# Kernel optimization log

Measured on AMD Instinct MI355X. Metric: run time of the kernel, lower is better.

## Reference

```python
import jax, jax.numpy as jnp
import numpy as np

TAU = 0.1
NEG = -1000000.0

def setup_inputs() -> dict:
    key = jax.random.key(0)
    x = jax.random.normal(key, (16, 2048, 512), dtype=jnp.float32)
    return {"x": x}

def reference(x):
    # x: [B, S, D]
    d = x.shape[-1]
    scores = jnp.einsum('bsd,btd->bst', x, x) / jnp.sqrt(jnp.asarray(d, x.dtype))
    scores = jnp.where(scores > TAU, scores, jnp.asarray(NEG, x.dtype))
    weights = jax.nn.softmax(scores, axis=-1)          # [B, S, S]
    context = jnp.einsum('bst,btd->bsd', weights, x)   # [B, S, D]
    return (context, weights)
```

## Files before the change

### kernel.cpp

```cpp
#include <hip/hip_runtime.h>
#include <hip/hip_bf16.h>
#include <stdint.h>

#define B_ 16
#define S_ 2048
#define D_ 512
#define TAU 0.1f
#define SCALE 0.04419417382415922f
#define BM 128
#define BN 32

typedef __attribute__((ext_vector_type(8))) __bf16 bf16x8;
typedef __attribute__((ext_vector_type(4))) float f32x4;
typedef __attribute__((ext_vector_type(16))) float f32x16;
typedef __attribute__((ext_vector_type(8))) uint16_t u16x8;
typedef __attribute__((ext_vector_type(4))) uint16_t u16x4;

__device__ __forceinline__ uint16_t f2bf(float f) {
  __hip_bfloat16 h = __float2bfloat16(f);
  return __builtin_bit_cast(uint16_t, h);
}

__device__ __forceinline__ float bf2f(uint16_t u) {
  return __uint_as_float(((uint32_t)u) << 16);
}

__device__ __forceinline__ void g2lds16(void* lds, const void* g) {
  __builtin_amdgcn_global_load_lds(
      (const __attribute__((address_space(1))) unsigned int*)g,
      (__attribute__((address_space(3))) unsigned int*)lds, 16, 0, 0);
}

__global__ __launch_bounds__(256) void convert_kernel(
    const float* __restrict__ x, uint16_t* __restrict__ xbf,
    uint16_t* __restrict__ xt) {
  const int bid = blockIdx.x;
  const int b = bid >> 8;
  const int tt = (bid >> 3) & 31;
  const int dt = bid & 7;
  const int t0 = tt * 64, d0 = dt * 64;
  __shared__ uint16_t tile[64][72];
  const int tid = threadIdx.x;
  const float* xb = x + ((size_t)b * S_ + t0) * D_ + d0;

#pragma unroll
  for (int it = 0; it < 4; ++it) {
    int r = it * 16 + (tid >> 4);
    int c = (tid & 15) * 4;
    float4 v = *(const float4*)(xb + (size_t)r * D_ + c);
    tile[r][c + 0] = f2bf(v.x);
    tile[r][c + 1] = f2bf(v.y);
    tile[r][c + 2] = f2bf(v.z);
    tile[r][c + 3] = f2bf(v.w);
  }
  __syncthreads();

#pragma unroll
  for (int it = 0; it < 2; ++it) {
    int G = it * 256 + tid;
    int tl = G >> 3, gl = G & 7;
    int t = t0 + tl;
    int p = (d0 >> 3) + (gl ^ (t & 7));
    u16x8 v = *(const u16x8*)&tile[tl][gl * 8];
    *(u16x8*)((char*)xbf + (size_t)(b * S_ + t) * 1024 + p * 16) = v;
  }
#pragma unroll
  for (int it = 0; it < 2; ++it) {
    int G = it * 256 + tid;
    int dl = G >> 3, gl = G & 7;
    int d = d0 + dl;
    int p = (gl & ~3) | ((gl ^ (d & 3)) & 3);
    u16x8 v;
#pragma unroll
    for (int i = 0; i < 8; ++i) v[i] = tile[gl * 8 + i][dl];
    *(u16x8*)((char*)xt + (size_t)(b * D_ + d) * 4096 + t0 * 2 + p * 16) = v;
  }
}

__global__ __launch_bounds__(512, 2) void attn_scores(
    const uint16_t* __restrict__ xbf, uint16_t* __restrict__ E,
    float* __restrict__ psum_g) {
  __shared__ uint16_t klds[64 * 512];
  __shared__ uint16_t wlds[4 * 32 * 64];
  __shared__ float redbuf[4 * 2 * 32];

  const int tid = threadIdx.x;
  const int wave = tid >> 6, lane = tid & 63;
  const int h = lane >> 5, l31 = lane & 31, l7 = lane & 7;
  const int qi = wave >> 1, ki = wave & 1;
  const int bid = blockIdx.x;
  const int job = (bid & 7) * 32 + (bid >> 3);
  const int b = job >> 4;
  const int q0 = (job & 15) * BM;

  const char* xb = (const char*)xbf + (size_t)b * S_ * 1024;
  const char* kldsc = (const char*)klds;
  char* wldsc = (char*)wlds;

  const size_t qrow = (size_t)(q0 + qi * 32 + l31);
  bf16x8 qf[32];
#pragma unroll
  for (int s = 0; s < 32; ++s) {
    int g = (2 * s + h) ^ l7;
    qf[s] = *(const bf16x8*)(xb + qrow * 1024 + g * 16);
  }

  float psum = 0.f;

  for (int kt = 0; kt < 32; ++kt) {
#pragma unroll
    for (int i = 0; i < 8; ++i) {
      int row = wave * 8 + i;
      g2lds16((char*)klds + row * 1024,
              xb + (size_t)(kt * 64 + row) * 1024 + lane * 16);
    }
    __syncthreads();

    f32x16 acc = {};
#pragma unroll
    for (int s = 0; s < 32; ++s) {
      int g = (2 * s + h) ^ l7;
      bf16x8 af = *(const bf16x8*)(kldsc + (size_t)(ki * 32 + l31) * 1024 + g * 16);
      acc = __builtin_amdgcn_mfma_f32_32x32x16_bf16(af, qf[s], acc, 0, 0, 0);
    }

#pragma unroll
    for (int rp = 0; rp < 8; ++rp) {
      int r = 2 * rp;
      float s0 = acc[r] * SCALE;
      float s1 = acc[r + 1] * SCALE;
      float e0 = (s0 > TAU) ? __expf(s0) : 0.f;
      float e1 = (s1 > TAU) ? __expf(s1) : 0.f;
      psum += e0 + e1;
      int k0 = ki * 32 + (r & 3) + 8 * (r >> 2) + 4 * h;
      int slot = (k0 >> 3) ^ l7;
      uint32_t pk = (uint32_t)f2bf(e0) | ((uint32_t)f2bf(e1) << 16);
      *(uint32_t*)(wldsc + qi * 4096 + l31 * 128 + slot * 16 + (k0 & 7) * 2) = pk;
    }
    __syncthreads();

#pragma unroll
    for (int j = 0; j < 2; ++j) {
      int ql = ki * 16 + j * 8 + (lane >> 3);
      u16x8 v = *(const u16x8*)(wldsc + qi * 4096 + ql * 128 + ((l7 ^ (ql & 7)) * 16));
      *(u16x8*)(E + ((size_t)(b * S_ + q0 + qi * 32 + ql)) * 2048 + kt * 64 + l7 * 8) = v;
    }
  }

  psum += __shfl_xor(psum, 32, 64);
  if (lane < 32) redbuf[qi * 64 + ki * 32 + lane] = psum;
  __syncthreads();
  if (ki == 0 && lane < 32) {
    float tot = redbuf[qi * 64 + lane] + redbuf[qi * 64 + 32 + lane];
    psum_g[(size_t)b * S_ + q0 + qi * 32 + lane] = tot;
  }
}

__global__ __launch_bounds__(512) void attn_pv3(
    const uint16_t* __restrict__ E, const uint16_t* __restrict__ xt,
    const float* __restrict__ psum_g, float* __restrict__ ctx,
    float* __restrict__ wout) {
  __shared__ uint16_t xtlds[2][512 * 64];
  __shared__ uint16_t wstage[128 * 64];
  __shared__ float invlds[128];

  const int tid = threadIdx.x;
  const int wave = tid >> 6, lane = tid & 63;
  const int h = lane >> 5, l31 = lane & 31, l7 = lane & 7;
  const int qi = wave >> 1, di = wave & 1;
  const int bid = blockIdx.x;
  const int job = (bid & 7) * 32 + (bid >> 3);
  const int b = job >> 4;
  const int q0 = (job & 15) * BM;

  const char* xtb = (const char*)xt + (size_t)b * D_ * 4096;
  char* wstc = (char*)wstage;

  const float inv = 1.0f / psum_g[(size_t)b * S_ + q0 + qi * 32 + l31];
  if (tid < 128) invlds[tid] = 1.0f / psum_g[(size_t)b * S_ + q0 + tid];

#pragma unroll
  for (int i = 0; i < 8; ++i) {
    int d = wave * 64 + i * 8 + (lane >> 3);
    int gd = l7 ^ (d & 7);
    int p2 = (gd & ~3) | ((gd ^ (d & 3)) & 3);
    g2lds16((char*)xtlds[0] + (wave * 64 + i * 8) * 128,
            xtb + (size_t)d * 4096 + p2 * 16);
  }
  __syncthreads();

  f32x16 pv[8];
#pragma unroll
  for (int t = 0; t < 8; ++t) pv[t] = (f32x16){};

  const uint16_t* Erow =
      E + ((size_t)(b * S_ + q0 + qi * 32 + l31)) * 2048 + 8 * h;

  for (int kt = 0; kt < 32; ++kt) {
    const int cur = kt & 1;
    const char* xcur = (const char*)xtlds[cur];

    if (kt < 31) {
#pragma unroll
      for (int i = 0; i < 8; ++i) {
        int d = wave * 64 + i * 8 + (lane >> 3);
        int gd = l7 ^ (d & 7);
        int p2 = (gd & ~3) | ((gd ^ (d & 3)) & 3);
        g2lds16((char*)xtlds[cur ^ 1] + (wave * 64 + i * 8) * 128,
                xtb + (size_t)d * 4096 + (kt + 1) * 128 + p2 * 16);
      }
    }

    bf16x8 bfr[4];
#pragma unroll
    for (int ks = 0; ks < 4; ++ks) {
      bfr[ks] = *(const bf16x8*)(Erow + kt * 64 + 16 * ks);
    }

#pragma unroll
    for (int t = 0; t < 8; ++t) {
      int dl = di * 256 + t * 32 + l31;
#pragma unroll
      for (int ks = 0; ks < 4; ++ks) {
        int slot = (2 * ks + h) ^ (dl & 7);
        bf16x8 af = *(const bf16x8*)(xcur + (size_t)dl * 128 + slot * 16);
        pv[t] = __builtin_amdgcn_mfma_f32_32x32x16_bf16(af, bfr[ks], pv[t], 0, 0, 0);
      }
    }

    if (di == 0) {
      int q = qi * 32 + l31;
#pragma unroll
      for (int ks = 0; ks < 4; ++ks) {
        int g = (2 * ks + h) ^ (q & 7);
        *(u16x8*)(wstc + q * 128 + g * 16) = __builtin_bit_cast(u16x8, bfr[ks]);
      }
    }
    __syncthreads();

#pragma unroll
    for (int j = 0; j < 2; ++j) {
      int row = wave * 16 + j * 8 + (lane >> 3);
      float invq = invlds[row];
#pragma unroll
      for (int half = 0; half < 2; ++half) {
        int g = (half * 4 + (l7 >> 1)) ^ (row & 7);
        u16x4 ev = *(const u16x4*)(wstc + row * 128 + g * 16 + (l7 & 1) * 8);
        f32x4 w;
#pragma unroll
        for (int i = 0; i < 4; ++i) w[i] = bf2f(ev[i]) * invq;
        *(f32x4*)(wout + ((size_t)(b * S_ + q0 + row)) * 2048 + kt * 64 +
                  half * 32 + l7 * 4) = w;
      }
    }
    __syncthreads();
  }

  char* sbuf = (char*)xtlds[0] + wave * 4096;
#pragma unroll
  for (int t = 0; t < 8; ++t) {
#pragma unroll
    for (int rp = 0; rp < 8; ++rp) {
      int r = 2 * rp;
      int d0 = (r & 3) + 8 * (r >> 2) + 4 * h;
      int g = (d0 >> 2) ^ (l31 & 7);
      float2 v = make_float2(pv[t][r] * inv, pv[t][r + 1] * inv);
      *(float2*)(sbuf + l31 * 128 + g * 16 + (d0 & 3) * 4) = v;
    }
#pragma unroll
    for (int jj = 0; jj < 4; ++jj) {
      int row = jj * 8 + (lane >> 3);
      int g = l7 ^ (row & 7);
      f32x4 vv = *(const f32x4*)(sbuf + row * 128 + g * 16);
      *(f32x4*)(ctx + ((size_t)(b * S_ + q0 + qi * 32 + row)) * 512 +
                di * 256 + t * 32 + l7 * 4) = vv;
    }
  }
}

__global__ __launch_bounds__(512, 2) void attn_main(
    const uint16_t* __restrict__ xbf, const uint16_t* __restrict__ xtr,
    float* __restrict__ ctx, float* __restrict__ wout) {
  __shared__ uint16_t klds[BN * D_];
  __shared__ uint16_t xtlds[D_ * BN];
  __shared__ uint16_t wlds[8][16][40];

  const int tid = threadIdx.x;
  const int wave = tid >> 6, lane = tid & 63;
  const int lg = lane >> 4, lr = lane & 15;
  const int bid = blockIdx.x;
  const int job = (bid & 7) * 32 + (bid >> 3);
  const int b = job >> 4;
  const int q0 = (job & 15) * BM;

  const char* xb = (const char*)(xbf + (size_t)b * S_ * D_);
  const char* xtb = (const char*)(xtr + (size_t)b * D_ * S_);

  const int qrow = q0 + wave * 16 + lr;
  bf16x8 qf[16];
#pragma unroll
  for (int c = 0; c < 16; ++c) {
    int g = (4 * c + lg) ^ (qrow & 7);
    qf[c] = *(const bf16x8*)(xb + (size_t)qrow * 1024 + g * 16);
  }

  float psum[4] = {0.f, 0.f, 0.f, 0.f};

  for (int kt = 0; kt < S_ / BN; ++kt) {
    const char* ksrc = xb + (size_t)kt * BN * 1024;
#pragma unroll
    for (int it = 0; it < 4; ++it) {
      int ob = it * 8192 + wave * 1024;
      g2lds16((char*)klds + ob, ksrc + ob + lane * 16);
    }
    __syncthreads();
    f32x4 acc0 = {0.f, 0.f, 0.f, 0.f}, acc1 = {0.f, 0.f, 0.f, 0.f};
#pragma unroll
    for (int c = 0; c < 16; ++c) {
      {
        int t = lr;
        int g = (4 * c + lg) ^ (t & 7);
        bf16x8 bf = *(const bf16x8*)((const char*)klds + t * 1024 + g * 16);
        acc0 = __builtin_amdgcn_mfma_f32_16x16x32_bf16(qf[c], bf, acc0, 0, 0, 0);
      }
      {
        int t = 16 + lr;
        int g = (4 * c + lg) ^ (t & 7);
        bf16x8 bf = *(const bf16x8*)((const char*)klds + t * 1024 + g * 16);
        acc1 = __builtin_amdgcn_mfma_f32_16x16x32_bf16(qf[c], bf, acc1, 0, 0, 0);
      }
    }
#pragma unroll
    for (int r = 0; r < 4; ++r) {
      float s0 = acc0[r] * SCALE;
      float s1 = acc1[r] * SCALE;
      psum[r] += (s0 > TAU ? __expf(s0) : 0.f) + (s1 > TAU ? __expf(s1) : 0.f);
    }
    __syncthreads();
  }

#pragma unroll
  for (int r = 0; r < 4; ++r) {
    float v = psum[r];
#pragma unroll
    for (int m = 1; m < 16; m <<= 1) v += __shfl_xor(v, m, 64);
    psum[r] = 1.f / v;
  }

  f32x4 pv[32];
  const f32x4 fz = {0.f, 0.f, 0.f, 0.f};
#pragma unroll
  for (int n = 0; n < 32; ++n) pv[n] = fz;

  for (int kt = 0; kt < S_ / BN; ++kt) {
    const char* ksrc = xb + (size_t)kt * BN * 1024;
#pragma unroll
    for (int it = 0; it < 4; ++it) {
      int ob = it * 8192 + wave * 1024;
      g2lds16((char*)klds + ob, ksrc + ob + lane * 16);
    }
#pragma unroll
    for (int it = 0; it < 4; ++it) {
      int ob = it * 8192 + wave * 1024;
      int o = ob + lane * 16;
      const char* src = xtb + (size_t)(o >> 6) * 4096 + kt * 64 + (o & 63);
      g2lds16((char*)xtlds + ob, src);
    }
    __syncthreads();

    f32x4 acc0 = {0.f, 0.f, 0.f, 0.f}, acc1 = {0.f, 0.f, 0.f, 0.f};
#pragma unroll
    for (int c = 0; c < 16; ++c) {
      {
        int t = lr;
        int g = (4 * c + lg) ^ (t & 7);
        bf16x8 bf = *(const bf16x8*)((const char*)klds + t * 1024 + g * 16);
        acc0 = __builtin_amdgcn_mfma_f32_16x16x32_bf16(qf[c], bf, acc0, 0, 0, 0);
      }
      {
        int t = 16 + lr;
        int g = (4 * c + lg) ^ (t & 7);
        bf16x8 bf = *(const bf16x8*)((const char*)klds + t * 1024 + g * 16);
        acc1 = __builtin_amdgcn_mfma_f32_16x16x32_bf16(qf[c], bf, acc1, 0, 0, 0);
      }
    }

#pragma unroll
    for (int j = 0; j < 2; ++j) {
      f32x4 a = j ? acc1 : acc0;
#pragma unroll
      for (int r = 0; r < 4; ++r) {
        float s = a[r] * SCALE;
        float w = (s > TAU) ? __expf(s) * psum[r] : 0.f;
        int ql = wave * 16 + 4 * lg + r;
        wout[((size_t)(b * S_ + q0 + ql)) * S_ + kt * BN + j * 16 + lr] = w;
        wlds[wave][4 * lg + r][j * 16 + lr] = f2bf(w);
      }
    }

    bf16x8 wa = *(const bf16x8*)((const char*)&wlds[wave][0][0] + lr * 80 + lg * 16);
#pragma unroll
    for (int n = 0; n < 32; ++n) {
      int d = n * 16 + lr;
      int g = lg ^ (d & 3);
      bf16x8 bf = *(const bf16x8*)((const char*)xtlds + d * 64 + g * 16);
      pv[n] = __builtin_amdgcn_mfma_f32_16x16x32_bf16(wa, bf, pv[n], 0, 0, 0);
    }
    __syncthreads();
  }

  const int qg = q0 + wave * 16 + 4 * lg;
#pragma unroll
  for (int n = 0; n < 32; ++n) {
#pragma unroll
    for (int r = 0; r < 4; ++r) {
      ctx[((size_t)(b * S_ + qg + r)) * D_ + n * 16 + lr] = pv[n][r];
    }
  }
}

__global__ __launch_bounds__(256) void fb_weights(const float* __restrict__ x,
                                                  float* __restrict__ wout) {
  const int b = blockIdx.x >> 11;
  const int q = blockIdx.x & 2047;
  __shared__ float qv[512];
  __shared__ float red[256];
  const int tid = threadIdx.x;
  const float* xb = x + (size_t)b * S_ * D_;
  for (int d = tid; d < 512; d += 256) qv[d] = xb[(size_t)q * 512 + d];
  __syncthreads();
  float s[8];
  float lsum = 0.f;
#pragma unroll
  for (int i = 0; i < 8; ++i) {
    int k = i * 256 + tid;
    const float* xr = xb + (size_t)k * 512;
    float dot = 0.f;
    for (int d = 0; d < 512; ++d) dot += qv[d] * xr[d];
    dot *= SCALE;
    float e = (dot > TAU) ? __expf(dot) : 0.f;
    s[i] = e;
    lsum += e;
  }
  red[tid] = lsum;
  __syncthreads();
  for (int st = 128; st > 0; st >>= 1) {
    if (tid < st) red[tid] += red[tid + st];
    __syncthreads();
  }
  float inv = 1.f / red[0];
#pragma unroll
  for (int i = 0; i < 8; ++i)
    wout[((size_t)(b * S_ + q)) * S_ + i * 256 + tid] = s[i] * inv;
}

__global__ __launch_bounds__(256) void fb_ctx(const float* __restrict__ x,
                                              const float* __restrict__ wout,
                                              float* __restrict__ ctx) {
  const int b = blockIdx.x >> 11;
  const int q = blockIdx.x & 2047;
  const int tid = threadIdx.x;
  const float* xb = x + (size_t)b * S_ * D_;
  const float* wr = wout + ((size_t)(b * S_ + q)) * S_;
  float a0 = 0.f, a1 = 0.f;
  for (int k = 0; k < 2048; ++k) {
    float w = wr[k];
    a0 += w * xb[(size_t)k * 512 + tid];
    a1 += w * xb[(size_t)k * 512 + 256 + tid];
  }
  ctx[((size_t)(b * S_ + q)) * 512 + tid] = a0;
  ctx[((size_t)(b * S_ + q)) * 512 + 256 + tid] = a1;
}

extern "C" void kernel_launch(void* const* d_in, const int* in_sizes, int n_in,
                              void* d_out, int out_size, void* d_ws, size_t ws_size,
                              hipStream_t stream) {
  (void)in_sizes; (void)n_in; (void)out_size;
  const float* x = (const float*)d_in[0];
  float* ctx = (float*)d_out;
  float* wout = (float*)d_out + (size_t)B_ * S_ * D_;

  const size_t half = (size_t)B_ * S_ * D_ * 2;
  const size_t e_bytes = (size_t)B_ * S_ * S_ * 2;
  const size_t psum_bytes = (size_t)B_ * S_ * 4;
  const size_t need_new = 2 * half + e_bytes + psum_bytes;

  if (ws_size >= need_new) {
    uint16_t* xbf = (uint16_t*)d_ws;
    uint16_t* xtr = (uint16_t*)((char*)d_ws + half);
    uint16_t* E = (uint16_t*)((char*)d_ws + 2 * half);
    float* psum_g = (float*)((char*)d_ws + 2 * half + e_bytes);
    convert_kernel<<<dim3(4096), dim3(256), 0, stream>>>(x, xbf, xtr);
    attn_scores<<<dim3(256), dim3(512), 0, stream>>>(xbf, E, psum_g);
    attn_pv3<<<dim3(256), dim3(512), 0, stream>>>(E, xtr, psum_g, ctx, wout);
  } else if (ws_size >= 2 * half) {
    uint16_t* xbf = (uint16_t*)d_ws;
    uint16_t* xtr = (uint16_t*)((char*)d_ws + half);
    convert_kernel<<<dim3(4096), dim3(256), 0, stream>>>(x, xbf, xtr);
    attn_main<<<dim3(256), dim3(512), 0, stream>>>(xbf, xtr, ctx, wout);
  } else {
    fb_weights<<<dim3(32768), dim3(256), 0, stream>>>(x, wout);
    fb_ctx<<<dim3(32768), dim3(256), 0, stream>>>(x, wout, ctx);
  }
}
```

Before: 292.7 us.

## Double-buffer K tiles in scores, write E and weights directly from registers

The scores kernel now double-buffers the K tile in LDS, prefetching the next tile during the MFMAs, and writes the bf16 exp values straight from accumulator registers to global memory instead of staging them through LDS. This removes one barrier and an LDS round trip per iteration. The PV kernel is remapped so each wave computes two 32-row query groups over 128 d columns, reusing each LDS A-fragment for two MFMAs. It writes normalized weights and context directly from registers without LDS staging. The direct global writes are narrower (8–16 byte) and less coalesced, and the register-held accumulators and fragments grow with the two-per-SM occupancy hint.

```diff
diff --git a/kernel.cpp b/kernel.cpp
--- a/kernel.cpp
+++ b/kernel.cpp
@@ -80,8 +80,7 @@
 __global__ __launch_bounds__(512, 2) void attn_scores(
     const uint16_t* __restrict__ xbf, uint16_t* __restrict__ E,
     float* __restrict__ psum_g) {
-  __shared__ uint16_t klds[64 * 512];
-  __shared__ uint16_t wlds[4 * 32 * 64];
+  __shared__ uint16_t klds[2][64 * 512];
   __shared__ float redbuf[4 * 2 * 32];
 
   const int tid = threadIdx.x;
@@ -94,8 +93,6 @@
   const int q0 = (job & 15) * BM;
 
   const char* xb = (const char*)xbf + (size_t)b * S_ * 1024;
-  const char* kldsc = (const char*)klds;
-  char* wldsc = (char*)wlds;
 
   const size_t qrow = (size_t)(q0 + qi * 32 + l31);
   bf16x8 qf[32];
@@ -107,14 +104,25 @@
 
   float psum = 0.f;
 
+#pragma unroll
+  for (int i = 0; i < 8; ++i) {
+    int row = wave * 8 + i;
+    g2lds16((char*)klds[0] + row * 1024, xb + (size_t)row * 1024 + lane * 16);
+  }
+  __syncthreads();
+
   for (int kt = 0; kt < 32; ++kt) {
-#pragma unroll
-    for (int i = 0; i < 8; ++i) {
-      int row = wave * 8 + i;
-      g2lds16((char*)klds + row * 1024,
-              xb + (size_t)(kt * 64 + row) * 1024 + lane * 16);
-    }
-    __syncthreads();
+    const int cur = kt & 1;
+    const char* kldsc = (const char*)klds[cur];
+
+    if (kt < 31) {
+#pragma unroll
+      for (int i = 0; i < 8; ++i) {
+        int row = wave * 8 + i;
+        g2lds16((char*)klds[cur ^ 1] + row * 1024,
+                xb + (size_t)((kt + 1) * 64 + row) * 1024 + lane * 16);
+      }
+    }
 
     f32x16 acc = {};
 #pragma unroll
@@ -124,27 +132,20 @@
       acc = __builtin_amdgcn_mfma_f32_32x32x16_bf16(af, qf[s], acc, 0, 0, 0);
     }
 
-#pragma unroll
-    for (int rp = 0; rp < 8; ++rp) {
-      int r = 2 * rp;
-      float s0 = acc[r] * SCALE;
-      float s1 = acc[r + 1] * SCALE;
-      float e0 = (s0 > TAU) ? __expf(s0) : 0.f;
-      float e1 = (s1 > TAU) ? __expf(s1) : 0.f;
-      psum += e0 + e1;
-      int k0 = ki * 32 + (r & 3) + 8 * (r >> 2) + 4 * h;
-      int slot = (k0 >> 3) ^ l7;
-      uint32_t pk = (uint32_t)f2bf(e0) | ((uint32_t)f2bf(e1) << 16);
-      *(uint32_t*)(wldsc + qi * 4096 + l31 * 128 + slot * 16 + (k0 & 7) * 2) = pk;
-    }
-    __syncthreads();
-
-#pragma unroll
-    for (int j = 0; j < 2; ++j) {
-      int ql = ki * 16 + j * 8 + (lane >> 3);
-      u16x8 v = *(const u16x8*)(wldsc + qi * 4096 + ql * 128 + ((l7 ^ (ql & 7)) * 16));
-      *(u16x8*)(E + ((size_t)(b * S_ + q0 + qi * 32 + ql)) * 2048 + kt * 64 + l7 * 8) = v;
-    }
+    uint16_t* ep = E + ((size_t)b * S_ + qrow) * 2048 + kt * 64 + ki * 32 + 4 * h;
+#pragma unroll
+    for (int q4 = 0; q4 < 4; ++q4) {
+      u16x4 w4;
+#pragma unroll
+      for (int j = 0; j < 4; ++j) {
+        float s = acc[4 * q4 + j] * SCALE;
+        float e = (s > TAU) ? __expf(s) : 0.f;
+        psum += e;
+        w4[j] = f2bf(e);
+      }
+      *(u16x4*)(ep + 8 * q4) = w4;
+    }
+    __syncthreads();
   }
 
   psum += __shfl_xor(psum, 32, 64);
@@ -156,28 +157,32 @@
   }
 }
 
-__global__ __launch_bounds__(512) void attn_pv3(
+__global__ __launch_bounds__(512, 2) void attn_pv5(
     const uint16_t* __restrict__ E, const uint16_t* __restrict__ xt,
     const float* __restrict__ psum_g, float* __restrict__ ctx,
     float* __restrict__ wout) {
   __shared__ uint16_t xtlds[2][512 * 64];
-  __shared__ uint16_t wstage[128 * 64];
-  __shared__ float invlds[128];
 
   const int tid = threadIdx.x;
   const int wave = tid >> 6, lane = tid & 63;
   const int h = lane >> 5, l31 = lane & 31, l7 = lane & 7;
-  const int qi = wave >> 1, di = wave & 1;
+  const int qi = wave & 1, di = wave >> 1;
   const int bid = blockIdx.x;
   const int job = (bid & 7) * 32 + (bid >> 3);
   const int b = job >> 4;
   const int q0 = (job & 15) * BM;
 
   const char* xtb = (const char*)xt + (size_t)b * D_ * 4096;
-  char* wstc = (char*)wstage;
-
-  const float inv = 1.0f / psum_g[(size_t)b * S_ + q0 + qi * 32 + l31];
-  if (tid < 128) invlds[tid] = 1.0f / psum_g[(size_t)b * S_ + q0 + tid];
+
+  float invq[2];
+#pragma unroll
+  for (int qg = 0; qg < 2; ++qg)
+    invq[qg] = 1.0f / psum_g[(size_t)b * S_ + q0 + qi * 64 + qg * 32 + l31];
+
+  const uint16_t* Erow[2];
+#pragma unroll
+  for (int qg = 0; qg < 2; ++qg)
+    Erow[qg] = E + ((size_t)(b * S_ + q0 + qi * 64 + qg * 32 + l31)) * 2048 + 8 * h;
 
 #pragma unroll
   for (int i = 0; i < 8; ++i) {
@@ -189,12 +194,11 @@
   }
   __syncthreads();
 
-  f32x16 pv[8];
-#pragma unroll
-  for (int t = 0; t < 8; ++t) pv[t] = (f32x16){};
-
-  const uint16_t* Erow =
-      E + ((size_t)(b * S_ + q0 + qi * 32 + l31)) * 2048 + 8 * h;
+  f32x16 pv[2][4];
+#pragma unroll
+  for (int qg = 0; qg < 2; ++qg)
+#pragma unroll
+    for (int t = 0; t < 4; ++t) pv[qg][t] = (f32x16){};
 
   for (int kt = 0; kt < 32; ++kt) {
     const int cur = kt & 1;
@@ -211,69 +215,57 @@
       }
     }
 
-    bf16x8 bfr[4];
-#pragma unroll
-    for (int ks = 0; ks < 4; ++ks) {
-      bfr[ks] = *(const bf16x8*)(Erow + kt * 64 + 16 * ks);
-    }
-
-#pragma unroll
-    for (int t = 0; t < 8; ++t) {
-      int dl = di * 256 + t * 32 + l31;
+    bf16x8 bfr[2][4];
+#pragma unroll
+    for (int qg = 0; qg < 2; ++qg)
+#pragma unroll
+      for (int ks = 0; ks < 4; ++ks)
+        bfr[qg][ks] = *(const bf16x8*)(Erow[qg] + kt * 64 + 16 * ks);
+
+#pragma unroll
+    for (int t = 0; t < 4; ++t) {
+      const int dl = di * 128 + t * 32 + l31;
 #pragma unroll
       for (int ks = 0; ks < 4; ++ks) {
-        int slot = (2 * ks + h) ^ (dl & 7);
+        int slot = (2 * ks + h) ^ l7;
         bf16x8 af = *(const bf16x8*)(xcur + (size_t)dl * 128 + slot * 16);
-        pv[t] = __builtin_amdgcn_mfma_f32_32x32x16_bf16(af, bfr[ks], pv[t], 0, 0, 0);
-      }
-    }
-
-    if (di == 0) {
-      int q = qi * 32 + l31;
+        pv[0][t] = __builtin_amdgcn_mfma_f32_32x32x16_bf16(af, bfr[0][ks], pv[0][t], 0, 0, 0);
+        pv[1][t] = __builtin_amdgcn_mfma_f32_32x32x16_bf16(af, bfr[1][ks], pv[1][t], 0, 0, 0);
+      }
+    }
+
+#pragma unroll
+    for (int qg = 0; qg < 2; ++qg) {
+      float* wp = wout + ((size_t)(b * S_ + q0 + qi * 64 + qg * 32 + l31)) * 2048 +
+                  kt * 64 + 8 * h;
 #pragma unroll
       for (int ks = 0; ks < 4; ++ks) {
-        int g = (2 * ks + h) ^ (q & 7);
-        *(u16x8*)(wstc + q * 128 + g * 16) = __builtin_bit_cast(u16x8, bfr[ks]);
-      }
-    }
-    __syncthreads();
-
-#pragma unroll
-    for (int j = 0; j < 2; ++j) {
-      int row = wave * 16 + j * 8 + (lane >> 3);
-      float invq = invlds[row];
-#pragma unroll
-      for (int half = 0; half < 2; ++half) {
-        int g = (half * 4 + (l7 >> 1)) ^ (row & 7);
-        u16x4 ev = *(const u16x4*)(wstc + row * 128 + g * 16 + (l7 & 1) * 8);
-        f32x4 w;
-#pragma unroll
-        for (int i = 0; i < 4; ++i) w[i] = bf2f(ev[i]) * invq;
-        *(f32x4*)(wout + ((size_t)(b * S_ + q0 + row)) * 2048 + kt * 64 +
-                  half * 32 + l7 * 4) = w;
-      }
-    }
-    __syncthreads();
-  }
-
-  char* sbuf = (char*)xtlds[0] + wave * 4096;
-#pragma unroll
-  for (int t = 0; t < 8; ++t) {
-#pragma unroll
-    for (int rp = 0; rp < 8; ++rp) {
-      int r = 2 * rp;
-      int d0 = (r & 3) + 8 * (r >> 2) + 4 * h;
-      int g = (d0 >> 2) ^ (l31 & 7);
-      float2 v = make_float2(pv[t][r] * inv, pv[t][r + 1] * inv);
-      *(float2*)(sbuf + l31 * 128 + g * 16 + (d0 & 3) * 4) = v;
-    }
-#pragma unroll
-    for (int jj = 0; jj < 4; ++jj) {
-      int row = jj * 8 + (lane >> 3);
-      int g = l7 ^ (row & 7);
-      f32x4 vv = *(const f32x4*)(sbuf + row * 128 + g * 16);
-      *(f32x4*)(ctx + ((size_t)(b * S_ + q0 + qi * 32 + row)) * 512 +
-                di * 256 + t * 32 + l7 * 4) = vv;
+        u16x8 ev = __builtin_bit_cast(u16x8, bfr[qg][ks]);
+        f32x4 w0, w1;
+#pragma unroll
+        for (int i = 0; i < 4; ++i) w0[i] = bf2f(ev[i]) * invq[qg];
+#pragma unroll
+        for (int i = 0; i < 4; ++i) w1[i] = bf2f(ev[4 + i]) * invq[qg];
+        *(f32x4*)(wp + 16 * ks) = w0;
+        *(f32x4*)(wp + 16 * ks + 4) = w1;
+      }
+    }
+    __syncthreads();
+  }
+
+#pragma unroll
+  for (int qg = 0; qg < 2; ++qg) {
+    float* cp = ctx + ((size_t)(b * S_ + q0 + qi * 64 + qg * 32 + l31)) * 512 +
+                di * 128 + 4 * h;
+#pragma unroll
+    for (int t = 0; t < 4; ++t) {
+#pragma unroll
+      for (int q4 = 0; q4 < 4; ++q4) {
+        f32x4 v;
+#pragma unroll
+        for (int j = 0; j < 4; ++j) v[j] = pv[qg][t][4 * q4 + j] * invq[qg];
+        *(f32x4*)(cp + t * 32 + 8 * q4) = v;
+      }
     }
   }
 }
@@ -492,7 +484,7 @@
     float* psum_g = (float*)((char*)d_ws + 2 * half + e_bytes);
     convert_kernel<<<dim3(4096), dim3(256), 0, stream>>>(x, xbf, xtr);
     attn_scores<<<dim3(256), dim3(512), 0, stream>>>(xbf, E, psum_g);
-    attn_pv3<<<dim3(256), dim3(512), 0, stream>>>(E, xtr, psum_g, ctx, wout);
+    attn_pv5<<<dim3(256), dim3(512), 0, stream>>>(E, xtr, psum_g, ctx, wout);
   } else if (ws_size >= 2 * half) {
     uint16_t* xbf = (uint16_t*)d_ws;
     uint16_t* xtr = (uint16_t*)((char*)d_ws + half);
```

After: 488.5 us. 1.67x slower.

## Double-buffer K tiles in scores kernel and prefetch E rows in PV kernel

Applied to the files above, without the earlier changes.

The scores kernel now double-buffers the K tile in LDS, issuing the next tile's async loads before the MFMA loop, and drops the LDS staging of exp weights. Each lane now writes its bf16 exp values straight to E as 8-byte stores. The PV kernel unrolls the k-loop by two with ping-pong register buffers so the next E fragment is loaded from global memory while the current one feeds MFMAs. The goal is to hide global load latency and remove an LDS round trip and one barrier per step. The cost is doubled LDS in the scores kernel (which may reduce occupancy at 2 blocks/CU), less coalesced E stores, and more registers in the PV kernel.

```diff
diff --git a/kernel.cpp b/kernel.cpp
--- a/kernel.cpp
+++ b/kernel.cpp
@@ -80,8 +80,7 @@
 __global__ __launch_bounds__(512, 2) void attn_scores(
     const uint16_t* __restrict__ xbf, uint16_t* __restrict__ E,
     float* __restrict__ psum_g) {
-  __shared__ uint16_t klds[64 * 512];
-  __shared__ uint16_t wlds[4 * 32 * 64];
+  __shared__ uint16_t klds[2][64 * 512];
   __shared__ float redbuf[4 * 2 * 32];
 
   const int tid = threadIdx.x;
@@ -94,8 +93,6 @@
   const int q0 = (job & 15) * BM;
 
   const char* xb = (const char*)xbf + (size_t)b * S_ * 1024;
-  const char* kldsc = (const char*)klds;
-  char* wldsc = (char*)wlds;
 
   const size_t qrow = (size_t)(q0 + qi * 32 + l31);
   bf16x8 qf[32];
@@ -107,14 +104,25 @@
 
   float psum = 0.f;
 
+#pragma unroll
+  for (int i = 0; i < 8; ++i) {
+    int row = wave * 8 + i;
+    g2lds16((char*)klds[0] + row * 1024, xb + (size_t)row * 1024 + lane * 16);
+  }
+  __syncthreads();
+
   for (int kt = 0; kt < 32; ++kt) {
-#pragma unroll
-    for (int i = 0; i < 8; ++i) {
-      int row = wave * 8 + i;
-      g2lds16((char*)klds + row * 1024,
-              xb + (size_t)(kt * 64 + row) * 1024 + lane * 16);
-    }
-    __syncthreads();
+    const int cur = kt & 1;
+    const char* kldsc = (const char*)klds[cur];
+
+    if (kt < 31) {
+#pragma unroll
+      for (int i = 0; i < 8; ++i) {
+        int row = wave * 8 + i;
+        g2lds16((char*)klds[cur ^ 1] + row * 1024,
+                xb + (size_t)((kt + 1) * 64 + row) * 1024 + lane * 16);
+      }
+    }
 
     f32x16 acc = {};
 #pragma unroll
@@ -124,27 +132,20 @@
       acc = __builtin_amdgcn_mfma_f32_32x32x16_bf16(af, qf[s], acc, 0, 0, 0);
     }
 
-#pragma unroll
-    for (int rp = 0; rp < 8; ++rp) {
-      int r = 2 * rp;
-      float s0 = acc[r] * SCALE;
-      float s1 = acc[r + 1] * SCALE;
-      float e0 = (s0 > TAU) ? __expf(s0) : 0.f;
-      float e1 = (s1 > TAU) ? __expf(s1) : 0.f;
-      psum += e0 + e1;
-      int k0 = ki * 32 + (r & 3) + 8 * (r >> 2) + 4 * h;
-      int slot = (k0 >> 3) ^ l7;
-      uint32_t pk = (uint32_t)f2bf(e0) | ((uint32_t)f2bf(e1) << 16);
-      *(uint32_t*)(wldsc + qi * 4096 + l31 * 128 + slot * 16 + (k0 & 7) * 2) = pk;
+    uint16_t* ep = E + ((size_t)b * S_ + qrow) * 2048 + kt * 64 + ki * 32 + 4 * h;
+#pragma unroll
+    for (int q4 = 0; q4 < 4; ++q4) {
+      u16x4 w4;
+#pragma unroll
+      for (int j = 0; j < 4; ++j) {
+        float s = acc[4 * q4 + j] * SCALE;
+        float e = (s > TAU) ? __expf(s) : 0.f;
+        psum += e;
+        w4[j] = f2bf(e);
+      }
+      *(u16x4*)(ep + 8 * q4) = w4;
     }
     __syncthreads();
-
-#pragma unroll
-    for (int j = 0; j < 2; ++j) {
-      int ql = ki * 16 + j * 8 + (lane >> 3);
-      u16x8 v = *(const u16x8*)(wldsc + qi * 4096 + ql * 128 + ((l7 ^ (ql & 7)) * 16));
-      *(u16x8*)(E + ((size_t)(b * S_ + q0 + qi * 32 + ql)) * 2048 + kt * 64 + l7 * 8) = v;
-    }
   }
 
   psum += __shfl_xor(psum, 32, 64);
@@ -156,7 +157,59 @@
   }
 }
 
-__global__ __launch_bounds__(512) void attn_pv3(
+#define PV_KT_BODY(KT, XCUR, XNXT, BCUR, BNXT)                                  \
+  do {                                                                          \
+    if ((KT) < 31) {                                                            \
+                         \
+      _Pragma("unroll") for (int ks = 0; ks < 4; ++ks)                          \
+          BNXT[ks] = *(const bf16x8*)(Erow + ((KT) + 1) * 64 + 16 * ks);        \
+                                  \
+      _Pragma("unroll") for (int i = 0; i < 8; ++i) {                           \
+        int d = wave * 64 + i * 8 + (lane >> 3);                                \
+        int gd = l7 ^ (d & 7);                                                  \
+        int p2 = (gd & ~3) | ((gd ^ (d & 3)) & 3);                              \
+        g2lds16((char*)(XNXT) + (wave * 64 + i * 8) * 128,                      \
+                xtb + (size_t)d * 4096 + ((KT) + 1) * 128 + p2 * 16);           \
+      }                                                                         \
+    }                                                                           \
+              \
+    _Pragma("unroll") for (int t = 0; t < 8; ++t) {                             \
+      int dl = di * 256 + t * 32 + l31;                                         \
+      _Pragma("unroll") for (int ks = 0; ks < 4; ++ks) {                        \
+        int slot = (2 * ks + h) ^ (dl & 7);                                     \
+        bf16x8 af =                                                             \
+            *(const bf16x8*)((const char*)(XCUR) + (size_t)dl * 128 + slot * 16);\
+        pv[t] = __builtin_amdgcn_mfma_f32_32x32x16_bf16(af, BCUR[ks], pv[t],    \
+                                                        0, 0, 0);               \
+      }                                                                         \
+    }                                                                           \
+             \
+    if (di == 0) {                                                              \
+      int q = qi * 32 + l31;                                                    \
+      _Pragma("unroll") for (int ks = 0; ks < 4; ++ks) {                        \
+        int g = (2 * ks + h) ^ (q & 7);                                         \
+        *(u16x8*)(wstc + q * 128 + g * 16) = __builtin_bit_cast(u16x8, BCUR[ks]);\
+      }                                                                         \
+    }                                                                           \
+    __syncthreads();                                                            \
+                  \
+    _Pragma("unroll") for (int j = 0; j < 2; ++j) {                             \
+      int row = wave * 16 + j * 8 + (lane >> 3);                                \
+      float invq = invlds[row];                                                 \
+      _Pragma("unroll") for (int hf = 0; hf < 2; ++hf) {                        \
+        int g = (hf * 4 + (l7 >> 1)) ^ (row & 7);                               \
+        u16x4 ev = *(const u16x4*)(wstc + row * 128 + g * 16 + (l7 & 1) * 8);   \
+        f32x4 w;                                                                \
+        _Pragma("unroll") for (int i2 = 0; i2 < 4; ++i2)                        \
+            w[i2] = bf2f(ev[i2]) * invq;                                        \
+        *(f32x4*)(wout + ((size_t)(b * S_ + q0 + row)) * 2048 + (KT) * 64 +     \
+                  hf * 32 + l7 * 4) = w;                                        \
+      }                                                                         \
+    }                                                                           \
+    __syncthreads();                                                            \
+  } while (0)
+
+__global__ __launch_bounds__(512) void attn_pv10(
     const uint16_t* __restrict__ E, const uint16_t* __restrict__ xt,
     const float* __restrict__ psum_g, float* __restrict__ ctx,
     float* __restrict__ wout) {
@@ -179,6 +232,12 @@
   const float inv = 1.0f / psum_g[(size_t)b * S_ + q0 + qi * 32 + l31];
   if (tid < 128) invlds[tid] = 1.0f / psum_g[(size_t)b * S_ + q0 + tid];
 
+  const uint16_t* Erow =
+      E + ((size_t)(b * S_ + q0 + qi * 32 + l31)) * 2048 + 8 * h;
+
+  bf16x8 bfrA[4], bfrB[4];
+#pragma unroll
+  for (int ks = 0; ks < 4; ++ks) bfrA[ks] = *(const bf16x8*)(Erow + 16 * ks);
 #pragma unroll
   for (int i = 0; i < 8; ++i) {
     int d = wave * 64 + i * 8 + (lane >> 3);
@@ -193,67 +252,9 @@
 #pragma unroll
   for (int t = 0; t < 8; ++t) pv[t] = (f32x16){};
 
-  const uint16_t* Erow =
-      E + ((size_t)(b * S_ + q0 + qi * 32 + l31)) * 2048 + 8 * h;
-
-  for (int kt = 0; kt < 32; ++kt) {
-    const int cur = kt & 1;
-    const char* xcur = (const char*)xtlds[cur];
-
-    if (kt < 31) {
-#pragma unroll
-      for (int i = 0; i < 8; ++i) {
-        int d = wave * 64 + i * 8 + (lane >> 3);
-        int gd = l7 ^ (d & 7);
-        int p2 = (gd & ~3) | ((gd ^ (d & 3)) & 3);
-        g2lds16((char*)xtlds[cur ^ 1] + (wave * 64 + i * 8) * 128,
-                xtb + (size_t)d * 4096 + (kt + 1) * 128 + p2 * 16);
-      }
-    }
-
-    bf16x8 bfr[4];
-#pragma unroll
-    for (int ks = 0; ks < 4; ++ks) {
-      bfr[ks] = *(const bf16x8*)(Erow + kt * 64 + 16 * ks);
-    }
-
-#pragma unroll
-    for (int t = 0; t < 8; ++t) {
-      int dl = di * 256 + t * 32 + l31;
-#pragma unroll
-      for (int ks = 0; ks < 4; ++ks) {
-        int slot = (2 * ks + h) ^ (dl & 7);
-        bf16x8 af = *(const bf16x8*)(xcur + (size_t)dl * 128 + slot * 16);
-        pv[t] = __builtin_amdgcn_mfma_f32_32x32x16_bf16(af, bfr[ks], pv[t], 0, 0, 0);
-      }
-    }
-
-    if (di == 0) {
-      int q = qi * 32 + l31;
-#pragma unroll
-      for (int ks = 0; ks < 4; ++ks) {
-        int g = (2 * ks + h) ^ (q & 7);
-        *(u16x8*)(wstc + q * 128 + g * 16) = __builtin_bit_cast(u16x8, bfr[ks]);
-      }
-    }
-    __syncthreads();
-
-#pragma unroll
-    for (int j = 0; j < 2; ++j) {
-      int row = wave * 16 + j * 8 + (lane >> 3);
-      float invq = invlds[row];
-#pragma unroll
-      for (int half = 0; half < 2; ++half) {
-        int g = (half * 4 + (l7 >> 1)) ^ (row & 7);
-        u16x4 ev = *(const u16x4*)(wstc + row * 128 + g * 16 + (l7 & 1) * 8);
-        f32x4 w;
-#pragma unroll
-        for (int i = 0; i < 4; ++i) w[i] = bf2f(ev[i]) * invq;
-        *(f32x4*)(wout + ((size_t)(b * S_ + q0 + row)) * 2048 + kt * 64 +
-                  half * 32 + l7 * 4) = w;
-      }
-    }
-    __syncthreads();
+  for (int kt = 0; kt < 32; kt += 2) {
+    PV_KT_BODY(kt, xtlds[0], xtlds[1], bfrA, bfrB);
+    PV_KT_BODY(kt + 1, xtlds[1], xtlds[0], bfrB, bfrA);
   }
 
   char* sbuf = (char*)xtlds[0] + wave * 4096;
@@ -492,7 +493,7 @@
     float* psum_g = (float*)((char*)d_ws + 2 * half + e_bytes);
     convert_kernel<<<dim3(4096), dim3(256), 0, stream>>>(x, xbf, xtr);
     attn_scores<<<dim3(256), dim3(512), 0, stream>>>(xbf, E, psum_g);
-    attn_pv3<<<dim3(256), dim3(512), 0, stream>>>(E, xtr, psum_g, ctx, wout);
+    attn_pv10<<<dim3(256), dim3(512), 0, stream>>>(E, xtr, psum_g, ctx, wout);
   } else if (ws_size >= 2 * half) {
     uint16_t* xbf = (uint16_t*)d_ws;
     uint16_t* xtr = (uint16_t*)((char*)d_ws + half);
```

New measurement: 281.6 us, median of 2. 3.8% less time.
